# Kernel optimization log

Measured on AMD Instinct MI355X. Metric: run time of the kernel, lower is better.

Reference implementation:

```python
import jax, jax.numpy as jnp
import numpy as np

H, HD, NKV = 16, 128, 4           # heads, head_dim, n_kv_heads (kv_groups=4)
SEL_TOPK, SEL_DIM, SEL_HEADS = 64, 64, 1
ROPE_BASE = 10000.0


def _rope_emb(t, hd):
    inv = 1.0 / (ROPE_BASE ** (jnp.arange(0, hd, 2, dtype=jnp.float32) / hd))
    freqs = jnp.arange(t, dtype=jnp.float32)[:, None] * inv[None, :]
    return jnp.concatenate([freqs, freqs], axis=-1)  # [t, hd]


def _apply_rotary(x, rope):
    # x: [b, t, h, hd]; rope: [t, hd] (rot_dim == hd here)
    cos = jnp.cos(rope)[None, :, None, :]
    sin = jnp.sin(rope)[None, :, None, :]
    x1, x2 = x[..., ::2], x[..., 1::2]
    c, s = cos[..., ::2], sin[..., ::2]
    rot = jnp.stack([x1 * c - x2 * s, x1 * s + x2 * c], axis=-1)
    return rot.reshape(x.shape)


def _selector_mask(q, k):
    # q, k: [b, H, t, hd] in UNrotated form (selector_rope='none'); causal=True
    b, h, t, d = q.shape
    qs = q[:, :SEL_HEADS, :, :SEL_DIM]
    ks = k[:, :SEL_HEADS, :, :SEL_DIM]
    scores = jnp.einsum('bhqd,bhkd->bhqk', qs, ks) / np.sqrt(SEL_DIM).astype(np.float32)
    future = jnp.triu(jnp.ones((t, t), bool), 1)
    scores = jnp.where(future[None, None], -jnp.inf, scores)
    idx = jax.lax.top_k(scores, SEL_TOPK)[1]  # [b, h_sel, t, keep]
    rows = jnp.arange(t)
    scatter_row = lambda im: jnp.zeros((t, t), bool).at[rows[:, None], im].set(True)
    sel = jax.vmap(jax.vmap(scatter_row))(idx)          # [b, h_sel, t, t]
    sel = sel.at[:, :, rows, rows].set(True)            # diagonal always kept
    sel = sel & jnp.tril(jnp.ones((t, t), bool))[None, None]
    sel = jnp.any(sel, axis=1, keepdims=True)           # h_sel < h -> broadcast mask
    return jnp.where(sel, 0.0, -jnp.inf).astype(jnp.float32)


def reference(x, Wq, bq, Wkd, bkd, Wku, bku, Wo, bo):
    b, t, d = x.shape
    G = H // NKV
    q = (x @ Wq + bq).reshape(b, t, H, HD)
    kv = (x @ Wkd + bkd) @ Wku + bku                    # MLA: down then up projection
    k = kv[..., : NKV * HD].reshape(b, t, NKV, HD)
    v = kv[..., NKV * HD:].reshape(b, t, NKV, HD)
    rope = _rope_emb(t, HD)
    qb = _apply_rotary(q, rope).transpose(0, 2, 1, 3)                     # [b,H,t,hd]
    kb = jnp.repeat(_apply_rotary(k, rope).transpose(0, 2, 1, 3), G, 1)   # GQA expand
    vb = jnp.repeat(v.transpose(0, 2, 1, 3), G, 1)
    # selector mask from unrotated q/k, detached (selector_detach=True)
    qu = jax.lax.stop_gradient(q.transpose(0, 2, 1, 3))
    ku = jnp.repeat(jax.lax.stop_gradient(k.transpose(0, 2, 1, 3)), G, 1)
    mask = _selector_mask(qu, ku)                                         # [b,1,t,t]
    scores = jnp.einsum('bhqd,bhkd->bhqk', qb, kb) / np.sqrt(HD).astype(np.float32)
    attn = jax.nn.softmax(scores + mask, axis=-1)
    y = jnp.einsum('bhqk,bhkd->bhqd', attn, vb)
    y = y.transpose(0, 2, 1, 3).reshape(b, t, H * HD)
    return y @ Wo + bo


def setup_inputs() -> dict:
    key = jax.random.key(0)
    ks = jax.random.split(key, 6)
    B, T, D, LAT = 2, 2048, 2048, 512
    s = 0.02
    return {
        'x': jax.random.normal(ks[0], (B, T, D), jnp.float32),
        'Wq': jax.random.normal(ks[1], (D, H * HD), jnp.float32) * s,
        'bq': jnp.zeros((H * HD,), jnp.float32),
        'Wkd': jax.random.normal(ks[2], (D, LAT), jnp.float32) * s,
        'bkd': jnp.zeros((LAT,), jnp.float32),
        'Wku': jax.random.normal(ks[3], (LAT, 2 * NKV * HD), jnp.float32) * s,
        'bku': jnp.zeros((2 * NKV * HD,), jnp.float32),
        'Wo': jax.random.normal(ks[4], (H * HD, D), jnp.float32) * s,
        'bo': jnp.zeros((D,), jnp.float32),
    }
```

## Files before the change

kernel.cpp:

```cpp
#include <hip/hip_runtime.h>

typedef unsigned int u32;
typedef unsigned long long u64;
typedef _Float16 f16;
typedef __attribute__((ext_vector_type(2))) _Float16 f16x2;
typedef __attribute__((ext_vector_type(4))) _Float16 f16x4;
typedef __attribute__((ext_vector_type(8))) _Float16 f16x8;
typedef __attribute__((ext_vector_type(4))) float f32x4;
typedef __attribute__((ext_vector_type(2))) double f64x2;


__device__ __forceinline__ int suX(int jj) { return jj ^ ((jj >> 4) & 7); }

__global__ __launch_bounds__(256) void k_transpose_cast(const float* __restrict__ in,
                                                        f16* __restrict__ out, int R, int C)
{
  __shared__ float tile[32][33];
  int c0 = blockIdx.x * 32, r0 = blockIdx.y * 32;
  int tx = threadIdx.x & 31, ty = threadIdx.x >> 5;
  #pragma unroll
  for (int i = ty; i < 32; i += 8) tile[i][tx] = in[(size_t)(r0 + i) * C + c0 + tx];
  __syncthreads();
  #pragma unroll
  for (int i = ty; i < 32; i += 8) out[(size_t)(c0 + i) * R + r0 + tx] = (f16)tile[tx][i];
}

__global__ __launch_bounds__(256) void k_cast_f16(const float* __restrict__ in,
                                                  f16* __restrict__ out, int n4)
{
  int i = blockIdx.x * 256 + threadIdx.x;
  if (i >= n4) return;
  f32x4 v = *(const f32x4*)&in[(size_t)i * 4];
  f16x4 h; h.x = (f16)v.x; h.y = (f16)v.y; h.z = (f16)v.z; h.w = (f16)v.w;
  *(f16x4*)&out[(size_t)i * 4] = h;
}

__global__ void k_prep_sel(const float* __restrict__ Wq, const float* __restrict__ Wkd,
                           const float* __restrict__ Wku, double* __restrict__ Bsel)
{
  const int k = blockIdx.x;
  const int j = threadIdx.x;
  Bsel[(size_t)k * 128 + j] = (double)Wq[(size_t)k * 2048 + j];
  double s = 0.0;
  for (int l = 0; l < 512; ++l)
    s = fma((double)Wkd[(size_t)k * 512 + l], (double)Wku[(size_t)l * 1024 + j], s);
  Bsel[(size_t)k * 128 + 64 + j] = s;
}

__global__ void k_bias_sel(const float* __restrict__ bq, const float* __restrict__ bkd,
                           const float* __restrict__ Wku, const float* __restrict__ bku,
                           double* __restrict__ bsel)
{
  int j = threadIdx.x;
  if (j < 64) {
    bsel[j] = (double)bq[j];
  } else {
    int jj = j - 64;
    double s = (double)bku[jj];
    for (int l = 0; l < 512; ++l)
      s = fma((double)bkd[l], (double)Wku[(size_t)l * 1024 + jj], s);
    bsel[j] = s;
  }
}

__global__ __launch_bounds__(256) void k_gemm_sel_f64(const float* __restrict__ A,
                                                      const double* __restrict__ Bsel,
                                                      double* __restrict__ partial)
{
  __shared__ double As[32][33];
  __shared__ double Bs[32][66];
  const int m0 = blockIdx.x * 32, n0 = blockIdx.y * 64;
  const int kbase = blockIdx.z * 512, kend = kbase + 512;
  const int tid = threadIdx.x;
  const int tx = tid & 15, ty = tid >> 4;
  const int ar = tid >> 3, ac4 = (tid & 7) * 4;
  double acc[2][4] = {};

  f32x4 aN = *(const f32x4*)&A[(size_t)(m0 + ar) * 2048 + kbase + ac4];
  f64x2 bN[4];
  #pragma unroll
  for (int it = 0; it < 4; ++it) {
    int c = it * 256 + tid; int kk = c >> 5, n2 = (c & 31) * 2;
    bN[it] = *(const f64x2*)&Bsel[(size_t)(kbase + kk) * 128 + n0 + n2];
  }
  for (int k0 = kbase; k0 < kend; k0 += 32) {
    __syncthreads();
    As[ar][ac4] = (double)aN.x; As[ar][ac4 + 1] = (double)aN.y;
    As[ar][ac4 + 2] = (double)aN.z; As[ar][ac4 + 3] = (double)aN.w;
    #pragma unroll
    for (int it = 0; it < 4; ++it) {
      int c = it * 256 + tid; int kk = c >> 5, n2 = (c & 31) * 2;
      Bs[kk][n2] = bN[it].x; Bs[kk][n2 + 1] = bN[it].y;
    }
    __syncthreads();
    if (k0 + 32 < kend) {
      aN = *(const f32x4*)&A[(size_t)(m0 + ar) * 2048 + k0 + 32 + ac4];
      #pragma unroll
      for (int it = 0; it < 4; ++it) {
        int c = it * 256 + tid; int kk = c >> 5, n2 = (c & 31) * 2;
        bN[it] = *(const f64x2*)&Bsel[(size_t)(k0 + 32 + kk) * 128 + n0 + n2];
      }
    }
    #pragma unroll
    for (int kk = 0; kk < 32; ++kk) {
      double a0 = As[ty * 2][kk], a1 = As[ty * 2 + 1][kk];
      f64x2 b01 = *(const f64x2*)&Bs[kk][tx * 4];
      f64x2 b23 = *(const f64x2*)&Bs[kk][tx * 4 + 2];
      acc[0][0] = fma(a0, b01.x, acc[0][0]); acc[0][1] = fma(a0, b01.y, acc[0][1]);
      acc[0][2] = fma(a0, b23.x, acc[0][2]); acc[0][3] = fma(a0, b23.y, acc[0][3]);
      acc[1][0] = fma(a1, b01.x, acc[1][0]); acc[1][1] = fma(a1, b01.y, acc[1][1]);
      acc[1][2] = fma(a1, b23.x, acc[1][2]); acc[1][3] = fma(a1, b23.y, acc[1][3]);
    }
  }
  double* op = partial + (size_t)blockIdx.z * 4096 * 128;
  #pragma unroll
  for (int i = 0; i < 2; ++i) {
    int row = m0 + ty * 2 + i;
    #pragma unroll
    for (int j = 0; j < 4; ++j) {
      int n = n0 + tx * 4 + j;
      op[(size_t)row * 128 + n] = acc[i][j];
    }
  }
}

__global__ __launch_bounds__(256) void k_sel_reduce(const double* __restrict__ partial,
                                                    const double* __restrict__ bias,
                                                    double* __restrict__ qs64,
                                                    double* __restrict__ ks64)
{
  const int idx = blockIdx.x * 256 + threadIdx.x;
  const int row = idx >> 7, n = idx & 127;
  const size_t S = 4096 * 128;
  double v = ((partial[idx] + partial[S + idx]) + partial[2 * S + idx]) + partial[3 * S + idx];
  v += bias[n];
  if (n < 64) qs64[(size_t)row * 64 + n] = v;
  else        ks64[(size_t)row * 64 + (n - 64)] = v;
}

__global__ __launch_bounds__(256) void k_transpose64(const double* __restrict__ in,
                                                     double* __restrict__ out)
{
  __shared__ double tile[32][33];
  const int bt = blockIdx.z;
  const int c0 = blockIdx.x * 32;
  const int r0 = blockIdx.y * 32;
  int tx = threadIdx.x & 31, ty = threadIdx.x >> 5;
  const double* ip = in + (size_t)bt * 2048 * 64;
  double* op = out + (size_t)bt * 64 * 2048;
  #pragma unroll
  for (int i = ty; i < 32; i += 8) tile[i][tx] = ip[(size_t)(r0 + i) * 64 + c0 + tx];
  __syncthreads();
  #pragma unroll
  for (int i = ty; i < 32; i += 8) op[(size_t)(c0 + i) * 2048 + r0 + tx] = tile[tx][i];
}

template <int MODE>
__global__ __launch_bounds__(256) void k_gemm_bt(const f16* __restrict__ A,
                                                 const f16* __restrict__ BT,
                                                 const float* __restrict__ bias,
                                                 float* __restrict__ C, f16* __restrict__ Ch,
                                                 f16* __restrict__ Kout, f16* __restrict__ Vout,
                                                 const float* __restrict__ rc,
                                                 const float* __restrict__ rs,
                                                 int M, int N, int K, int lda, int ldb, int ldc)
{
  __shared__ __align__(16) f16 As[128 * 64];
  __shared__ __align__(16) f16 Bs[128 * 64];
  const int tid = threadIdx.x;
  const int lane = tid & 63;
  const int wave = tid >> 6;
  int bx = blockIdx.x, by = blockIdx.y;
  {
    const int nwg = gridDim.x * gridDim.y;
    if ((nwg & 7) == 0) {
      const int bid = by * gridDim.x + bx;
      const int cpx = nwg >> 3;
      const int sbid = (bid & 7) * cpx + (bid >> 3);
      bx = sbid % gridDim.x;
      by = sbid / gridDim.x;
    }
  }
  const int m0 = bx * 128, n0 = by * 128;
  const int wr = (wave >> 1) * 64, wc = (wave & 1) * 64;
  const int lrow = lane & 15;
  const int kgrp = (lane >> 4) * 8;
  f32x4 acc[4][4] = {};

  for (int k0 = 0; k0 < K; k0 += 64) {
    __syncthreads();
    #pragma unroll
    for (int it = 0; it < 4; ++it) {
      int c = it * 256 + tid;
      int r = c >> 3, c8 = (c & 7) * 8;
      int lbase = (it * 256 + (tid & 192)) * 8;
      const f16* ga = A + (size_t)(m0 + r) * lda + k0 + c8;
      __builtin_amdgcn_global_load_lds((const __attribute__((address_space(1))) u32*)ga,
                                       (__attribute__((address_space(3))) u32*)&As[lbase],
                                       16, 0, 0);
      const f16* gb = BT + (size_t)(n0 + r) * ldb + k0 + c8;
      __builtin_amdgcn_global_load_lds((const __attribute__((address_space(1))) u32*)gb,
                                       (__attribute__((address_space(3))) u32*)&Bs[lbase],
                                       16, 0, 0);
    }
    __syncthreads();
    #pragma unroll
    for (int ks = 0; ks < 2; ++ks) {
      f16x8 af[4], bfr[4];
      #pragma unroll
      for (int m = 0; m < 4; ++m)
        af[m] = *(const f16x8*)&As[(wr + m * 16 + lrow) * 64 + ks * 32 + kgrp];
      #pragma unroll
      for (int n = 0; n < 4; ++n)
        bfr[n] = *(const f16x8*)&Bs[(wc + n * 16 + lrow) * 64 + ks * 32 + kgrp];
      #pragma unroll
      for (int m = 0; m < 4; ++m)
        #pragma unroll
        for (int n = 0; n < 4; ++n)
          acc[m][n] = __builtin_amdgcn_mfma_f32_16x16x32_f16(af[m], bfr[n], acc[m][n], 0, 0, 0);
    }
  }
  const int rbase = m0 + wr + (lane >> 4) * 4;
  #pragma unroll
  for (int n = 0; n < 4; ++n) {
    int col = n0 + wc + n * 16 + lrow;
    float bv = bias ? bias[col] : 0.0f;
    const int ri = (col & 127) >> 1;
    #pragma unroll
    for (int m = 0; m < 4; ++m) {
      #pragma unroll
      for (int j = 0; j < 4; ++j) {
        int rowi = rbase + m * 16 + j;
        float v = acc[m][n][j] + bv;
        if (MODE == 0) {
          C[(size_t)rowi * ldc + col] = v;
        } else if (MODE == 1) {
          Ch[(size_t)rowi * ldc + col] = (f16)v;
        } else if (MODE == 2) {
          float vp = __shfl_xor(v, 1);
          int t = rowi & 2047;
          float c_ = rc[t * 64 + ri], s_ = rs[t * 64 + ri];
          float r_ = (lrow & 1) ? (vp * s_ + v * c_) : (v * c_ - vp * s_);
          Ch[(size_t)rowi * ldc + col] = (f16)r_;
        } else {
          float vp = __shfl_xor(v, 1);
          if (n0 < 512) {
            int t = rowi & 2047;
            float c_ = rc[t * 64 + ri], s_ = rs[t * 64 + ri];
            float r_ = (lrow & 1) ? (vp * s_ + v * c_) : (v * c_ - vp * s_);
            Kout[(size_t)rowi * 512 + col] = (f16)r_;
          } else {
            Vout[(size_t)rowi * 512 + (col - 512)] = (f16)v;
          }
        }
      }
    }
  }
}

__global__ void k_rope_table(float* __restrict__ rc, float* __restrict__ rs)
{
  int t = blockIdx.x, i = threadIdx.x;
  int fi = (2 * i) & 63;
  double inv = pow(10000.0, -(double)fi / 64.0);
  double a = (double)t * inv;
  rc[t * 64 + i] = (float)cos(a);
  rs[t * 64 + i] = (float)sin(a);
}

__global__ __launch_bounds__(256) void k_topk64(const double* __restrict__ qs,
                                                const double* __restrict__ ksT,
                                                int* __restrict__ selcnt,
                                                int* __restrict__ selidx)
{
  const int r0 = blockIdx.x * 2;
  const int b = r0 >> 11;
  const int t0 = r0 & 2047, t1 = t0 + 1;
  const int tid = threadIdx.x;
  const int lane = tid & 63, wave = tid >> 6;
  if (t1 < 64) {
    for (int lr = 0; lr < 2; ++lr) {
      int t = t0 + lr;
      int* outp = selidx + (size_t)(r0 + lr) * 68;
      for (int jj = tid; jj <= t; jj += 256) outp[jj] = jj;
      if (tid == 0) selcnt[r0 + lr] = t + 1;
    }
    return;
  }
  __shared__ double qrowP[64][2];
  __shared__ u64 su[2][2048];
  __shared__ unsigned hist[256];
  __shared__ unsigned wsum[4];
  __shared__ unsigned s_bsel, s_larger, s_cnt;
  __shared__ u64 s_thr;
  __shared__ int s_remfin;
  __shared__ int cand[128];
  __shared__ u64 ckey[128];

  if (tid < 128) qrowP[tid >> 1][tid & 1] = qs[(size_t)(r0 + (tid & 1)) * 64 + (tid >> 1)];
  __syncthreads();
  {
    const double* kb = ksT + (size_t)b * 64 * 2048;
    const int emax = t1 >> 8;
    for (int e = 0; e <= emax; ++e) {
      const int jj = e * 256 + tid;
      const double* kp = kb + jj;
      double a0 = 0.0, a1 = 0.0, b0 = 0.0, b1 = 0.0;
      #pragma unroll 8
      for (int d = 0; d < 64; d += 2) {
        double kv0 = kp[(size_t)d * 2048];
        double kv1 = kp[(size_t)(d + 1) * 2048];
        f64x2 qp0 = *(const f64x2*)&qrowP[d][0];
        f64x2 qp1 = *(const f64x2*)&qrowP[d + 1][0];
        a0 = fma(qp0.x, kv0, a0); a1 = fma(qp0.y, kv0, a1);
        b0 = fma(qp1.x, kv1, b0); b1 = fma(qp1.y, kv1, b1);
      }
      const int sx = suX(jj);
      u64 u0 = (u64)__double_as_longlong(a0 + b0);
      su[0][sx] = (u0 >> 63) ? ~u0 : (u0 | 0x8000000000000000ull);
      u64 u1 = (u64)__double_as_longlong(a1 + b1);
      su[1][sx] = (u1 >> 63) ? ~u1 : (u1 | 0x8000000000000000ull);
    }
  }
  __syncthreads();

  const int c0 = tid * 8;
  for (int lr = 0; lr < 2; ++lr) {
    const int t = t0 + lr;
    int* outp = selidx + (size_t)(r0 + lr) * 68;
    const u64* S = su[lr];
    u64 prefix = 0;
    int remaining = 64;
    int broke = 0, sh_final = 0;
    for (int byte = 7; byte >= 0; --byte) {
      const int sh = byte * 8;
      hist[tid] = 0;
      __syncthreads();
      {
        unsigned bn[8]; bool vl[8];
        #pragma unroll
        for (int e = 0; e < 8; ++e) {
          int jj = c0 + e;
          u64 u = (jj <= t) ? S[suX(jj)] : 0;
          bool ok = (jj <= t) && ((byte == 7) || (((u ^ prefix) >> (sh + 8)) == 0));
          bn[e] = (unsigned)((u >> sh) & 255);
          vl[e] = ok;
        }
        #pragma unroll
        for (int e = 0; e < 8; ++e) {
          if (vl[e]) {
            bool first = true;
            #pragma unroll
            for (int p = 0; p < 8; ++p)
              if (p < e && vl[p] && bn[p] == bn[e]) first = false;
            if (first) {
              unsigned c = 0;
              #pragma unroll
              for (int q = 0; q < 8; ++q)
                if (q >= e && vl[q] && bn[q] == bn[e]) ++c;
              atomicAdd(&hist[bn[e]], c);
            }
          }
        }
      }
      __syncthreads();
      const unsigned h = hist[tid];
      unsigned v = h;
      #pragma unroll
      for (int off = 1; off < 64; off <<= 1) {
        unsigned tv = __shfl_down(v, off);
        if (lane + off < 64) v += tv;
      }
      if (lane == 0) wsum[wave] = v;
      __syncthreads();
      unsigned add = 0;
      #pragma unroll
      for (int w = 0; w < 4; ++w)
        if (w > wave) add += wsum[w];
      const unsigned inc = v + add;
      const unsigned cumAbove = inc - h;
      __syncthreads();
      if ((int)cumAbove < remaining && (int)inc >= remaining) {
        s_bsel = (unsigned)tid;
        s_larger = cumAbove;
        s_cnt = inc - cumAbove;
      }
      __syncthreads();
      prefix |= ((u64)s_bsel << sh);
      remaining -= (int)s_larger;
      int cnt = (int)s_cnt;
      if (cnt <= 128) { broke = 1; sh_final = sh; break; }
    }
    u64 thr;
    int remfin;
    if (broke) {
      unsigned cg = 0;
      #pragma unroll
      for (int e = 0; e < 8; ++e) {
        int jj = c0 + e;
        if (jj <= t && (((S[suX(jj)] ^ prefix) >> sh_final) == 0)) ++cg;
      }
      unsigned v = cg;
      #pragma unroll
      for (int off = 1; off < 64; off <<= 1) {
        unsigned tv = __shfl_up(v, off);
        if (lane >= off) v += tv;
      }
      __syncthreads();
      if (lane == 63) wsum[wave] = v;
      __syncthreads();
      unsigned add = 0, tot = 0;
      #pragma unroll
      for (int w = 0; w < 4; ++w) {
        tot += wsum[w];
        if (w < wave) add += wsum[w];
      }
      const int C = (int)tot;
      int pos = (int)(v + add - cg);
      __syncthreads();
      #pragma unroll
      for (int e = 0; e < 8; ++e) {
        int jj = c0 + e;
        if (jj <= t && (((S[suX(jj)] ^ prefix) >> sh_final) == 0)) cand[pos++] = jj;
      }
      __syncthreads();
      if (tid < C) ckey[tid] = S[suX(cand[tid])];
      __syncthreads();
      if (tid < C) {
        u64 k = ckey[tid];
        int g = 0, eq = 0;
        for (int j = 0; j < C; ++j) {
          g += (ckey[j] > k) ? 1 : 0;
          eq += (ckey[j] == k) ? 1 : 0;
        }
        if (g < remaining && remaining <= g + eq) {
          s_thr = k;
          s_remfin = remaining - g;
        }
      }
      __syncthreads();
      thr = s_thr;
      remfin = s_remfin;
    } else {
      thr = prefix;
      remfin = remaining;
    }
    __syncthreads();
    unsigned cg = 0, ct_ = 0;
    #pragma unroll
    for (int e = 0; e < 8; ++e) {
      int jj = c0 + e;
      if (jj <= t) {
        u64 u = S[suX(jj)];
        cg += (u > thr) ? 1u : 0u;
        ct_ += (u == thr) ? 1u : 0u;
      }
    }
    const unsigned pack = cg | (ct_ << 16);
    {
      unsigned v = pack;
      #pragma unroll
      for (int off = 1; off < 64; off <<= 1) {
        unsigned tv = __shfl_up(v, off);
        if (lane >= off) v += tv;
      }
      if (lane == 63) wsum[wave] = v;
      __syncthreads();
      unsigned add = 0, tot = 0;
      #pragma unroll
      for (int w = 0; w < 4; ++w) {
        tot += wsum[w];
        if (w < wave) add += wsum[w];
      }
      const unsigned excl = v + add - pack;
      __syncthreads();
      const unsigned Gtot = tot & 0xFFFFu;
      const u64 ut = S[suX(t)];
      const unsigned gt = (ut > thr) ? 1u : 0u;
      const unsigned tt = (ut == thr) ? 1u : 0u;
      const int GtotX = (int)(Gtot - gt);
      int gpos = (int)(excl & 0xFFFFu);
      int tpos = (int)(excl >> 16);
      #pragma unroll
      for (int e = 0; e < 8; ++e) {
        int jj = c0 + e;
        if (jj > t) break;
        u64 u = S[suX(jj)];
        if (u > thr) {
          if (jj != t) outp[1 + gpos] = jj;
          ++gpos;
        } else if (u == thr) {
          if (jj != t && tpos < remfin) outp[1 + GtotX + tpos] = jj;
          ++tpos;
        }
      }
      if (tid == 0) {
        outp[0] = t;
        const unsigned Ttot = tot >> 16;
        int tb = (int)(Ttot - tt);
        int emitT = tb < remfin ? tb : remfin;
        selcnt[r0 + lr] = 1 + GtotX + emitT;
      }
    }
    __syncthreads();
  }
}

__global__ __launch_bounds__(256) void k_attn(const f16* __restrict__ qr,
                                              const f16* __restrict__ kr,
                                              const f16* __restrict__ vv,
                                              const int* __restrict__ selcnt,
                                              const int* __restrict__ selidx,
                                              f16* __restrict__ y)
{
  const int blk = blockIdx.x;
  const int row = blk >> 2, kvh = blk & 3;
  const int b = row >> 11;
  const int tid = threadIdx.x, lane = tid & 63, wave = tid >> 6;
  const int cnt = selcnt[row];
  __shared__ int sidx[68];
  __shared__ __align__(16) f16 Kl[65 * 128];
  __shared__ __align__(16) f16 Vl[68 * 128];
  __shared__ f16 qlds[4][128];
  __shared__ __align__(4) f16 ph[4][72];
  if (tid < cnt) sidx[tid] = selidx[(size_t)row * 68 + tid];
  *(f16x2*)&qlds[wave][lane * 2] =
      *(const f16x2*)&qr[((size_t)row * 16 + kvh * 4 + wave) * 128 + lane * 2];
  __syncthreads();

  f16x8 kreg[5], vreg[5];
  int rr[5], cc[5]; bool vld[5];
  #pragma unroll
  for (int it = 0; it < 5; ++it) {
    const int c = it * 256 + tid;
    const int r = c >> 4, ch = c & 15;
    const bool ok = (r < cnt);
    const int rsafe = ok ? sidx[r] : sidx[0];
    const size_t kbase = ((size_t)(b * 2048 + rsafe)) * 512 + kvh * 128 + ch * 8;
    kreg[it] = *(const f16x8*)&kr[kbase];
    vreg[it] = *(const f16x8*)&vv[kbase];
    rr[it] = r; cc[it] = ch; vld[it] = ok;
  }
  #pragma unroll
  for (int it = 0; it < 5; ++it) {
    if (vld[it]) {
      *(f16x8*)&Kl[rr[it] * 128 + ((cc[it] ^ (rr[it] & 15)) * 8)] = kreg[it];
      *(f16x8*)&Vl[rr[it] * 128 + cc[it] * 8] = vreg[it];
    }
  }
  for (int i = tid; i < (68 - cnt) * 64; i += 256)
    ((u32*)Vl)[cnt * 64 + i] = 0u;
  __syncthreads();

  const float SCALE = 0.08838834764831845f;
  auto dotk = [&](int r) -> float {
    const int sw = r & 15;
    float s = 0.0f;
    #pragma unroll
    for (int i = 0; i < 16; ++i) {
      f16x8 k8 = *(const f16x8*)&Kl[r * 128 + ((i ^ sw) * 8)];
      f16x8 q8 = *(const f16x8*)&qlds[wave][i * 8];
      #pragma unroll
      for (int e = 0; e < 4; ++e) {
        f16x2 ka; ka.x = k8[2 * e]; ka.y = k8[2 * e + 1];
        f16x2 qa; qa.x = q8[2 * e]; qa.y = q8[2 * e + 1];
        s = __builtin_amdgcn_fdot2(ka, qa, s, false);
      }
    }
    return s * SCALE;
  };

  float s1 = -__builtin_inff(), s2 = -__builtin_inff();
  if (lane < cnt) s1 = dotk(lane);
  if (lane + 64 < cnt) s2 = dotk(lane + 64);
  float mx = fmaxf(s1, s2);
  #pragma unroll
  for (int off = 32; off; off >>= 1) mx = fmaxf(mx, __shfl_xor(mx, off));
  float p1 = (lane < cnt) ? __expf(s1 - mx) : 0.0f;
  float p2 = (lane + 64 < cnt) ? __expf(s2 - mx) : 0.0f;
  float l = p1 + p2;
  #pragma unroll
  for (int off = 32; off; off >>= 1) l += __shfl_xor(l, off);
  float linv = 1.0f / l;
  ph[wave][lane] = (f16)p1;
  if (lane == 0) ph[wave][64] = (f16)p2;
  if (lane >= 1 && lane < 8) ph[wave][64 + lane] = (f16)0.f;
  __syncthreads();

  float y0 = 0.0f, y1 = 0.0f;
  const int d2 = lane * 2;
  for (int j = 0; j < cnt; j += 2) {
    f16x2 pp = *(const f16x2*)&ph[wave][j];
    f16x2 va = *(const f16x2*)&Vl[(j + 0) * 128 + d2];
    f16x2 vb = *(const f16x2*)&Vl[(j + 1) * 128 + d2];
    f16x2 v0; v0.x = va.x; v0.y = vb.x;
    f16x2 v1; v1.x = va.y; v1.y = vb.y;
    y0 = __builtin_amdgcn_fdot2(pp, v0, y0, false);
    y1 = __builtin_amdgcn_fdot2(pp, v1, y1, false);
  }
  y0 *= linv; y1 *= linv;
  f16x2 o; o.x = (f16)y0; o.y = (f16)y1;
  *(f16x2*)&y[(size_t)row * 2048 + (kvh * 4 + wave) * 128 + d2] = o;
}

extern "C" void kernel_launch(void* const* d_in, const int* in_sizes, int n_in,
                              void* d_out, int out_size, void* d_ws, size_t ws_size,
                              hipStream_t stream)
{
  (void)in_sizes; (void)n_in; (void)out_size; (void)ws_size;
  const float* x   = (const float*)d_in[0];
  const float* Wq  = (const float*)d_in[1];
  const float* bq  = (const float*)d_in[2];
  const float* Wkd = (const float*)d_in[3];
  const float* bkd = (const float*)d_in[4];
  const float* Wku = (const float*)d_in[5];
  const float* bku = (const float*)d_in[6];
  const float* Wo  = (const float*)d_in[7];
  const float* bo  = (const float*)d_in[8];
  float* out = (float*)d_out;

  char* ws = (char*)d_ws;
  size_t o = 0;
  auto alloc = [&](size_t bytes) -> void* {
    o = (o + 255) & ~(size_t)255;
    void* p = ws + o;
    o += bytes;
    return p;
  };
  f16* WqT   = (f16*)alloc(2048ull * 2048 * 2);
  f16* WoT   = (f16*)alloc(2048ull * 2048 * 2);
  f16* WkdT  = (f16*)alloc(512ull * 2048 * 2);
  f16* WkuT  = (f16*)alloc(1024ull * 512 * 2);
  f16* xh    = (f16*)alloc(4096ull * 2048 * 2);
  f16* yh    = (f16*)alloc(4096ull * 2048 * 2);
  f16* cbf   = (f16*)alloc(4096ull * 512 * 2);
  float* rc  = (float*)alloc(2048ull * 64 * 4);
  float* rs  = (float*)alloc(2048ull * 64 * 4);
  f16* qrope = (f16*)alloc(4096ull * 2048 * 2);
  f16* krope = (f16*)alloc(4096ull * 512 * 2);
  f16* vbf   = (f16*)alloc(4096ull * 512 * 2);
  int* selcnt = (int*)alloc(4096ull * 4);
  int* selidx = (int*)alloc(4096ull * 68 * 4);
  double* Bsel = (double*)alloc(2048ull * 128 * 8);
  double* bsel = (double*)alloc(128 * 8);
  double* qs64 = (double*)alloc(4096ull * 64 * 8);
  double* ks64 = (double*)alloc(4096ull * 64 * 8);
  double* ksT  = (double*)alloc(2ull * 64 * 2048 * 8);
  double* partial = (double*)qrope;

  k_transpose_cast<<<dim3(64, 64), 256, 0, stream>>>(Wq, WqT, 2048, 2048);
  k_transpose_cast<<<dim3(16, 64), 256, 0, stream>>>(Wkd, WkdT, 2048, 512);
  k_transpose_cast<<<dim3(32, 16), 256, 0, stream>>>(Wku, WkuT, 512, 1024);
  k_transpose_cast<<<dim3(64, 64), 256, 0, stream>>>(Wo, WoT, 2048, 2048);
  k_cast_f16<<<8192, 256, 0, stream>>>(x, xh, 2097152);
  k_rope_table<<<2048, 64, 0, stream>>>(rc, rs);

  k_prep_sel<<<2048, 64, 0, stream>>>(Wq, Wkd, Wku, Bsel);
  k_bias_sel<<<1, 128, 0, stream>>>(bq, bkd, Wku, bku, bsel);
  k_gemm_sel_f64<<<dim3(128, 2, 4), 256, 0, stream>>>(x, Bsel, partial);
  k_sel_reduce<<<2048, 256, 0, stream>>>(partial, bsel, qs64, ks64);
  k_transpose64<<<dim3(2, 64, 2), 256, 0, stream>>>(ks64, ksT);

  k_gemm_bt<2><<<dim3(32, 16), 256, 0, stream>>>(xh, WqT, bq, nullptr, qrope,
                                                 nullptr, nullptr, rc, rs,
                                                 4096, 2048, 2048, 2048, 2048, 2048);
  k_gemm_bt<1><<<dim3(32, 4), 256, 0, stream>>>(xh, WkdT, bkd, nullptr, cbf,
                                                nullptr, nullptr, nullptr, nullptr,
                                                4096, 512, 2048, 2048, 2048, 512);
  k_gemm_bt<3><<<dim3(32, 8), 256, 0, stream>>>(cbf, WkuT, bku, nullptr, nullptr,
                                                krope, vbf, rc, rs,
                                                4096, 1024, 512, 512, 512, 1024);

  k_topk64<<<2048, 256, 0, stream>>>(qs64, ksT, selcnt, selidx);

  k_attn<<<16384, 256, 0, stream>>>(qrope, krope, vbf, selcnt, selidx, yh);

  k_gemm_bt<0><<<dim3(32, 16), 256, 0, stream>>>(yh, WoT, bo, out, nullptr,
                                                 nullptr, nullptr, nullptr, nullptr,
                                                 4096, 2048, 2048, 2048, 2048, 2048);
}
```

Baseline: 543.4 us.

## Horizontally fuse independent prep, GEMM and top-k kernels into combined launches

Independent kernels are merged into shared launches that dispatch on block index. The four weight transposes and the x cast become one kernel. The f64 selector GEMM runs alongside the KV down-projection, the selector reduce alongside the KV up-projection, and the Q projection alongside the top-k selection. This removes several launch gaps and lets small, under-filled kernels share the GPU with larger ones. In exchange, each fused kernel reserves the largest shared-memory footprint of its branches, which may lower occupancy for the GEMM blocks.

```diff
diff --git a/kernel.cpp b/kernel.cpp
--- a/kernel.cpp
+++ b/kernel.cpp
@@ -12,27 +12,45 @@
 
 __device__ __forceinline__ int suX(int jj) { return jj ^ ((jj >> 4) & 7); }
 
-__global__ __launch_bounds__(256) void k_transpose_cast(const float* __restrict__ in,
-                                                        f16* __restrict__ out, int R, int C)
-{
-  __shared__ float tile[32][33];
-  int c0 = blockIdx.x * 32, r0 = blockIdx.y * 32;
+__device__ __forceinline__ void dev_transpose_cast(char* smem, int bx, int by,
+                                                   const float* __restrict__ in,
+                                                   f16* __restrict__ out, int R, int C)
+{
+  float* tile = (float*)smem;
+  int c0 = bx * 32, r0 = by * 32;
   int tx = threadIdx.x & 31, ty = threadIdx.x >> 5;
   #pragma unroll
-  for (int i = ty; i < 32; i += 8) tile[i][tx] = in[(size_t)(r0 + i) * C + c0 + tx];
+  for (int i = ty; i < 32; i += 8) tile[i * 33 + tx] = in[(size_t)(r0 + i) * C + c0 + tx];
   __syncthreads();
   #pragma unroll
-  for (int i = ty; i < 32; i += 8) out[(size_t)(c0 + i) * R + r0 + tx] = (f16)tile[tx][i];
-}
-
-__global__ __launch_bounds__(256) void k_cast_f16(const float* __restrict__ in,
-                                                  f16* __restrict__ out, int n4)
-{
-  int i = blockIdx.x * 256 + threadIdx.x;
-  if (i >= n4) return;
-  f32x4 v = *(const f32x4*)&in[(size_t)i * 4];
-  f16x4 h; h.x = (f16)v.x; h.y = (f16)v.y; h.z = (f16)v.z; h.w = (f16)v.w;
-  *(f16x4*)&out[(size_t)i * 4] = h;
+  for (int i = ty; i < 32; i += 8) out[(size_t)(c0 + i) * R + r0 + tx] = (f16)tile[tx * 33 + i];
+}
+
+__global__ __launch_bounds__(256) void k_fusedP(const float* __restrict__ Wq, f16* __restrict__ WqT,
+                                                const float* __restrict__ Wkd, f16* __restrict__ WkdT,
+                                                const float* __restrict__ Wku, f16* __restrict__ WkuT,
+                                                const float* __restrict__ Wo, f16* __restrict__ WoT,
+                                                const float* __restrict__ x, f16* __restrict__ xh)
+{
+  __shared__ __align__(16) char smem[4224];
+  const int id = blockIdx.x;
+  if (id < 4096) {
+    dev_transpose_cast(smem, id & 63, id >> 6, Wq, WqT, 2048, 2048);
+  } else if (id < 5120) {
+    int g = id - 4096;
+    dev_transpose_cast(smem, g & 15, g >> 4, Wkd, WkdT, 2048, 512);
+  } else if (id < 5632) {
+    int g = id - 5120;
+    dev_transpose_cast(smem, g & 31, g >> 5, Wku, WkuT, 512, 1024);
+  } else if (id < 9728) {
+    int g = id - 5632;
+    dev_transpose_cast(smem, g & 63, g >> 6, Wo, WoT, 2048, 2048);
+  } else {
+    int i = (id - 9728) * 256 + threadIdx.x;
+    f32x4 v = *(const f32x4*)&x[(size_t)i * 4];
+    f16x4 h; h.x = (f16)v.x; h.y = (f16)v.y; h.z = (f16)v.z; h.w = (f16)v.w;
+    *(f16x4*)&xh[(size_t)i * 4] = h;
+  }
 }
 
 __global__ void k_prep_sel(const float* __restrict__ Wq, const float* __restrict__ Wkd,
@@ -63,14 +81,15 @@
   }
 }
 
-__global__ __launch_bounds__(256) void k_gemm_sel_f64(const float* __restrict__ A,
-                                                      const double* __restrict__ Bsel,
-                                                      double* __restrict__ partial)
-{
-  __shared__ double As[32][33];
-  __shared__ double Bs[32][66];
-  const int m0 = blockIdx.x * 32, n0 = blockIdx.y * 64;
-  const int kbase = blockIdx.z * 512, kend = kbase + 512;
+__device__ __forceinline__ void dev_sel_f64(char* smem, int bx, int by, int bz,
+                                            const float* __restrict__ A,
+                                            const double* __restrict__ Bsel,
+                                            double* __restrict__ partial)
+{
+  double* Asd = (double*)smem;
+  double* Bsd = (double*)smem + 32 * 33;
+  const int m0 = bx * 32, n0 = by * 64;
+  const int kbase = bz * 512, kend = kbase + 512;
   const int tid = threadIdx.x;
   const int tx = tid & 15, ty = tid >> 4;
   const int ar = tid >> 3, ac4 = (tid & 7) * 4;
@@ -85,12 +104,12 @@
   }
   for (int k0 = kbase; k0 < kend; k0 += 32) {
     __syncthreads();
-    As[ar][ac4] = (double)aN.x; As[ar][ac4 + 1] = (double)aN.y;
-    As[ar][ac4 + 2] = (double)aN.z; As[ar][ac4 + 3] = (double)aN.w;
+    Asd[ar * 33 + ac4] = (double)aN.x; Asd[ar * 33 + ac4 + 1] = (double)aN.y;
+    Asd[ar * 33 + ac4 + 2] = (double)aN.z; Asd[ar * 33 + ac4 + 3] = (double)aN.w;
     #pragma unroll
     for (int it = 0; it < 4; ++it) {
       int c = it * 256 + tid; int kk = c >> 5, n2 = (c & 31) * 2;
-      Bs[kk][n2] = bN[it].x; Bs[kk][n2 + 1] = bN[it].y;
+      Bsd[kk * 66 + n2] = bN[it].x; Bsd[kk * 66 + n2 + 1] = bN[it].y;
     }
     __syncthreads();
     if (k0 + 32 < kend) {
@@ -103,16 +122,16 @@
     }
     #pragma unroll
     for (int kk = 0; kk < 32; ++kk) {
-      double a0 = As[ty * 2][kk], a1 = As[ty * 2 + 1][kk];
-      f64x2 b01 = *(const f64x2*)&Bs[kk][tx * 4];
-      f64x2 b23 = *(const f64x2*)&Bs[kk][tx * 4 + 2];
+      double a0 = Asd[(ty * 2) * 33 + kk], a1 = Asd[(ty * 2 + 1) * 33 + kk];
+      f64x2 b01 = *(const f64x2*)&Bsd[kk * 66 + tx * 4];
+      f64x2 b23 = *(const f64x2*)&Bsd[kk * 66 + tx * 4 + 2];
       acc[0][0] = fma(a0, b01.x, acc[0][0]); acc[0][1] = fma(a0, b01.y, acc[0][1]);
       acc[0][2] = fma(a0, b23.x, acc[0][2]); acc[0][3] = fma(a0, b23.y, acc[0][3]);
       acc[1][0] = fma(a1, b01.x, acc[1][0]); acc[1][1] = fma(a1, b01.y, acc[1][1]);
       acc[1][2] = fma(a1, b23.x, acc[1][2]); acc[1][3] = fma(a1, b23.y, acc[1][3]);
     }
   }
-  double* op = partial + (size_t)blockIdx.z * 4096 * 128;
+  double* op = partial + (size_t)bz * 4096 * 128;
   #pragma unroll
   for (int i = 0; i < 2; ++i) {
     int row = m0 + ty * 2 + i;
@@ -124,12 +143,13 @@
   }
 }
 
-__global__ __launch_bounds__(256) void k_sel_reduce(const double* __restrict__ partial,
-                                                    const double* __restrict__ bias,
-                                                    double* __restrict__ qs64,
-                                                    double* __restrict__ ks64)
-{
-  const int idx = blockIdx.x * 256 + threadIdx.x;
+__device__ __forceinline__ void dev_sel_reduce(int blk,
+                                               const double* __restrict__ partial,
+                                               const double* __restrict__ bias,
+                                               double* __restrict__ qs64,
+                                               double* __restrict__ ks64)
+{
+  const int idx = blk * 256 + threadIdx.x;
   const int row = idx >> 7, n = idx & 127;
   const size_t S = 4096 * 128;
   double v = ((partial[idx] + partial[S + idx]) + partial[2 * S + idx]) + partial[3 * S + idx];
@@ -156,29 +176,30 @@
 }
 
 template <int MODE>
-__global__ __launch_bounds__(256) void k_gemm_bt(const f16* __restrict__ A,
-                                                 const f16* __restrict__ BT,
-                                                 const float* __restrict__ bias,
-                                                 float* __restrict__ C, f16* __restrict__ Ch,
-                                                 f16* __restrict__ Kout, f16* __restrict__ Vout,
-                                                 const float* __restrict__ rc,
-                                                 const float* __restrict__ rs,
-                                                 int M, int N, int K, int lda, int ldb, int ldc)
-{
-  __shared__ __align__(16) f16 As[128 * 64];
-  __shared__ __align__(16) f16 Bs[128 * 64];
+__device__ __forceinline__ void dev_gemm_bt(char* smem, int gbx, int gby, int nbx, int nby,
+                                            const f16* __restrict__ A,
+                                            const f16* __restrict__ BT,
+                                            const float* __restrict__ bias,
+                                            float* __restrict__ C, f16* __restrict__ Ch,
+                                            f16* __restrict__ Kout, f16* __restrict__ Vout,
+                                            const float* __restrict__ rc,
+                                            const float* __restrict__ rs,
+                                            int K, int lda, int ldb, int ldc)
+{
+  f16* As = (f16*)smem;
+  f16* Bs = (f16*)smem + 128 * 64;
   const int tid = threadIdx.x;
   const int lane = tid & 63;
   const int wave = tid >> 6;
-  int bx = blockIdx.x, by = blockIdx.y;
+  int bx = gbx, by = gby;
   {
-    const int nwg = gridDim.x * gridDim.y;
+    const int nwg = nbx * nby;
     if ((nwg & 7) == 0) {
-      const int bid = by * gridDim.x + bx;
+      const int bid = by * nbx + bx;
       const int cpx = nwg >> 3;
       const int sbid = (bid & 7) * cpx + (bid >> 3);
-      bx = sbid % gridDim.x;
-      by = sbid / gridDim.x;
+      bx = sbid % nbx;
+      by = sbid / nbx;
     }
   }
   const int m0 = bx * 128, n0 = by * 128;
@@ -268,12 +289,11 @@
   rs[t * 64 + i] = (float)sin(a);
 }
 
-__global__ __launch_bounds__(256) void k_topk64(const double* __restrict__ qs,
-                                                const double* __restrict__ ksT,
-                                                int* __restrict__ selcnt,
-                                                int* __restrict__ selidx)
-{
-  const int r0 = blockIdx.x * 2;
+__device__ void dev_topk64(char* smem, int blk,
+                           const double* __restrict__ qs, const double* __restrict__ ksT,
+                           int* __restrict__ selcnt, int* __restrict__ selidx)
+{
+  const int r0 = blk * 2;
   const int b = r0 >> 11;
   const int t0 = r0 & 2047, t1 = t0 + 1;
   const int tid = threadIdx.x;
@@ -287,17 +307,19 @@
     }
     return;
   }
-  __shared__ double qrowP[64][2];
-  __shared__ u64 su[2][2048];
-  __shared__ unsigned hist[256];
-  __shared__ unsigned wsum[4];
-  __shared__ unsigned s_bsel, s_larger, s_cnt;
-  __shared__ u64 s_thr;
-  __shared__ int s_remfin;
-  __shared__ int cand[128];
-  __shared__ u64 ckey[128];
-
-  if (tid < 128) qrowP[tid >> 1][tid & 1] = qs[(size_t)(r0 + (tid & 1)) * 64 + (tid >> 1)];
+  double* qrowP = (double*)smem;
+  u64* su = (u64*)(smem + 1024);
+  u64* ckey = (u64*)(smem + 33792);
+  u64* ps_thr = (u64*)(smem + 34816);
+  unsigned* hist = (unsigned*)(smem + 34824);
+  unsigned* wsum = (unsigned*)(smem + 35848);
+  unsigned* ps_bsel = (unsigned*)(smem + 35864);
+  unsigned* ps_larger = (unsigned*)(smem + 35868);
+  unsigned* ps_cnt = (unsigned*)(smem + 35872);
+  int* ps_remfin = (int*)(smem + 35876);
+  int* cand = (int*)(smem + 35880);
+
+  if (tid < 128) qrowP[(tid >> 1) * 2 + (tid & 1)] = qs[(size_t)(r0 + (tid & 1)) * 64 + (tid >> 1)];
   __syncthreads();
   {
     const double* kb = ksT + (size_t)b * 64 * 2048;
@@ -310,16 +332,16 @@
       for (int d = 0; d < 64; d += 2) {
         double kv0 = kp[(size_t)d * 2048];
         double kv1 = kp[(size_t)(d + 1) * 2048];
-        f64x2 qp0 = *(const f64x2*)&qrowP[d][0];
-        f64x2 qp1 = *(const f64x2*)&qrowP[d + 1][0];
+        f64x2 qp0 = *(const f64x2*)&qrowP[d * 2];
+        f64x2 qp1 = *(const f64x2*)&qrowP[(d + 1) * 2];
         a0 = fma(qp0.x, kv0, a0); a1 = fma(qp0.y, kv0, a1);
         b0 = fma(qp1.x, kv1, b0); b1 = fma(qp1.y, kv1, b1);
       }
       const int sx = suX(jj);
       u64 u0 = (u64)__double_as_longlong(a0 + b0);
-      su[0][sx] = (u0 >> 63) ? ~u0 : (u0 | 0x8000000000000000ull);
+      su[sx] = (u0 >> 63) ? ~u0 : (u0 | 0x8000000000000000ull);
       u64 u1 = (u64)__double_as_longlong(a1 + b1);
-      su[1][sx] = (u1 >> 63) ? ~u1 : (u1 | 0x8000000000000000ull);
+      su[2048 + sx] = (u1 >> 63) ? ~u1 : (u1 | 0x8000000000000000ull);
     }
   }
   __syncthreads();
@@ -328,7 +350,7 @@
   for (int lr = 0; lr < 2; ++lr) {
     const int t = t0 + lr;
     int* outp = selidx + (size_t)(r0 + lr) * 68;
-    const u64* S = su[lr];
+    const u64* S = su + lr * 2048;
     u64 prefix = 0;
     int remaining = 64;
     int broke = 0, sh_final = 0;
@@ -381,14 +403,14 @@
       const unsigned cumAbove = inc - h;
       __syncthreads();
       if ((int)cumAbove < remaining && (int)inc >= remaining) {
-        s_bsel = (unsigned)tid;
-        s_larger = cumAbove;
-        s_cnt = inc - cumAbove;
-      }
-      __syncthreads();
-      prefix |= ((u64)s_bsel << sh);
-      remaining -= (int)s_larger;
-      int cnt = (int)s_cnt;
+        *ps_bsel = (unsigned)tid;
+        *ps_larger = cumAbove;
+        *ps_cnt = inc - cumAbove;
+      }
+      __syncthreads();
+      prefix |= ((u64)(*ps_bsel) << sh);
+      remaining -= (int)(*ps_larger);
+      int cnt = (int)(*ps_cnt);
       if (cnt <= 128) { broke = 1; sh_final = sh; break; }
     }
     u64 thr;
@@ -434,13 +456,13 @@
           eq += (ckey[j] == k) ? 1 : 0;
         }
         if (g < remaining && remaining <= g + eq) {
-          s_thr = k;
-          s_remfin = remaining - g;
+          *ps_thr = k;
+          *ps_remfin = remaining - g;
         }
       }
       __syncthreads();
-      thr = s_thr;
-      remfin = s_remfin;
+      thr = *ps_thr;
+      remfin = *ps_remfin;
     } else {
       thr = prefix;
       remfin = remaining;
@@ -504,6 +526,77 @@
     }
     __syncthreads();
   }
+}
+
+__global__ __launch_bounds__(256) void k_fusedA(const float* __restrict__ x,
+                                                const double* __restrict__ Bsel,
+                                                double* __restrict__ partial,
+                                                const f16* __restrict__ xh,
+                                                const f16* __restrict__ WkdT,
+                                                const float* __restrict__ bkd,
+                                                f16* __restrict__ cbf)
+{
+  __shared__ __align__(16) char smem[32768];
+  const int id = blockIdx.x;
+  if (id < 1024) {
+    dev_sel_f64(smem, id & 127, (id >> 7) & 1, id >> 8, x, Bsel, partial);
+  } else {
+    const int g = id - 1024;
+    dev_gemm_bt<1>(smem, g & 31, g >> 5, 32, 4, xh, WkdT, bkd, nullptr, cbf,
+                   nullptr, nullptr, nullptr, nullptr, 2048, 2048, 2048, 512);
+  }
+}
+
+__global__ __launch_bounds__(256) void k_fusedC(const f16* __restrict__ cbf,
+                                                const f16* __restrict__ WkuT,
+                                                const float* __restrict__ bku,
+                                                f16* __restrict__ krope, f16* __restrict__ vbf,
+                                                const float* __restrict__ rc,
+                                                const float* __restrict__ rs,
+                                                const double* __restrict__ partial,
+                                                const double* __restrict__ bsel,
+                                                double* __restrict__ qs64,
+                                                double* __restrict__ ks64)
+{
+  __shared__ __align__(16) char smem[32768];
+  const int id = blockIdx.x;
+  if (id < 256) {
+    dev_gemm_bt<3>(smem, id & 31, id >> 5, 32, 8, cbf, WkuT, bku, nullptr, nullptr,
+                   krope, vbf, rc, rs, 512, 512, 512, 1024);
+  } else {
+    dev_sel_reduce(id - 256, partial, bsel, qs64, ks64);
+  }
+}
+
+__global__ __launch_bounds__(256) void k_fusedB(const f16* __restrict__ xh,
+                                                const f16* __restrict__ WqT,
+                                                const float* __restrict__ bq,
+                                                f16* __restrict__ qrope,
+                                                const float* __restrict__ rc,
+                                                const float* __restrict__ rs,
+                                                const double* __restrict__ qs64,
+                                                const double* __restrict__ ksT,
+                                                int* __restrict__ selcnt,
+                                                int* __restrict__ selidx)
+{
+  __shared__ __align__(16) char smem[36608];
+  const int id = blockIdx.x;
+  if (id < 512) {
+    dev_gemm_bt<2>(smem, id & 31, id >> 5, 32, 16, xh, WqT, bq, nullptr, qrope,
+                   nullptr, nullptr, rc, rs, 2048, 2048, 2048, 2048);
+  } else {
+    dev_topk64(smem, id - 512, qs64, ksT, selcnt, selidx);
+  }
+}
+
+__global__ __launch_bounds__(256) void k_gemm0(const f16* __restrict__ A,
+                                               const f16* __restrict__ BT,
+                                               const float* __restrict__ bias,
+                                               float* __restrict__ C)
+{
+  __shared__ __align__(16) char smem[32768];
+  dev_gemm_bt<0>(smem, blockIdx.x, blockIdx.y, 32, 16, A, BT, bias, C, nullptr,
+                 nullptr, nullptr, nullptr, nullptr, 2048, 2048, 2048, 2048);
 }
 
 __global__ __launch_bounds__(256) void k_attn(const f16* __restrict__ qr,
@@ -648,34 +741,22 @@
   double* ksT  = (double*)alloc(2ull * 64 * 2048 * 8);
   double* partial = (double*)qrope;
 
-  k_transpose_cast<<<dim3(64, 64), 256, 0, stream>>>(Wq, WqT, 2048, 2048);
-  k_transpose_cast<<<dim3(16, 64), 256, 0, stream>>>(Wkd, WkdT, 2048, 512);
-  k_transpose_cast<<<dim3(32, 16), 256, 0, stream>>>(Wku, WkuT, 512, 1024);
-  k_transpose_cast<<<dim3(64, 64), 256, 0, stream>>>(Wo, WoT, 2048, 2048);
-  k_cast_f16<<<8192, 256, 0, stream>>>(x, xh, 2097152);
-  k_rope_table<<<2048, 64, 0, stream>>>(rc, rs);
-
   k_prep_sel<<<2048, 64, 0, stream>>>(Wq, Wkd, Wku, Bsel);
   k_bias_sel<<<1, 128, 0, stream>>>(bq, bkd, Wku, bku, bsel);
-  k_gemm_sel_f64<<<dim3(128, 2, 4), 256, 0, stream>>>(x, Bsel, partial);
-  k_sel_reduce<<<2048, 256, 0, stream>>>(partial, bsel, qs64, ks64);
+  k_rope_table<<<2048, 64, 0, stream>>>(rc, rs);
+  k_fusedP<<<17920, 256, 0, stream>>>(Wq, WqT, Wkd, WkdT, Wku, WkuT, Wo, WoT, x, xh);
+
+  k_fusedA<<<1152, 256, 0, stream>>>(x, Bsel, partial, xh, WkdT, bkd, cbf);
+
+  k_fusedC<<<2304, 256, 0, stream>>>(cbf, WkuT, bku, krope, vbf, rc, rs,
+                                     partial, bsel, qs64, ks64);
+
   k_transpose64<<<dim3(2, 64, 2), 256, 0, stream>>>(ks64, ksT);
 
-  k_gemm_bt<2><<<dim3(32, 16), 256, 0, stream>>>(xh, WqT, bq, nullptr, qrope,
-                                                 nullptr, nullptr, rc, rs,
-                                                 4096, 2048, 2048, 2048, 2048, 2048);
-  k_gemm_bt<1><<<dim3(32, 4), 256, 0, stream>>>(xh, WkdT, bkd, nullptr, cbf,
-                                                nullptr, nullptr, nullptr, nullptr,
-                                                4096, 512, 2048, 2048, 2048, 512);
-  k_gemm_bt<3><<<dim3(32, 8), 256, 0, stream>>>(cbf, WkuT, bku, nullptr, nullptr,
-                                                krope, vbf, rc, rs,
-                                                4096, 1024, 512, 512, 512, 1024);
-
-  k_topk64<<<2048, 256, 0, stream>>>(qs64, ksT, selcnt, selidx);
+  k_fusedB<<<2560, 256, 0, stream>>>(xh, WqT, bq, qrope, rc, rs,
+                                     qs64, ksT, selcnt, selidx);
 
   k_attn<<<16384, 256, 0, stream>>>(qrope, krope, vbf, selcnt, selidx, yh);
 
-  k_gemm_bt<0><<<dim3(32, 16), 256, 0, stream>>>(yh, WoT, bo, out, nullptr,
-                                                 nullptr, nullptr, nullptr, nullptr,
-                                                 4096, 2048, 2048, 2048, 2048, 2048);
-}
+  k_gemm0<<<dim3(32, 16), 256, 0, stream>>>(yh, WoT, bo, out);
+}
```

Measured after the change: 542.3 us. No clear change (-0.2%).
